# Performance work log

Measured on AMD Instinct MI355X. Metric: run time of the kernel, lower is better.

The kernel has to match this reference:

```python
import jax, jax.numpy as jnp
import numpy as np

IDENTITY_WEIGHT = 0.5
EPS_NORM = 1e-6   # channel RMSNorm eps
EPS_COS = 1e-12   # cosine-sim norm eps (matches torch F.normalize default)


def setup_inputs() -> dict:
    key = jax.random.key(0)
    k1, k2 = jax.random.split(key)
    B, C, H, W = 32, 768, 32, 32
    X = jax.random.normal(k1, (B, C, H, W), dtype=jnp.float32)
    # 1x1 conv weight [out=3C, in=C] (kernel dims squeezed)
    W_in = jax.random.normal(k2, (3 * C, C), dtype=jnp.float32) * (C ** -0.5)
    return {"X": X, "W_in": W_in}


def _cos_sim(t):
    # normalize over the flattened spatial axis (last dim)
    return t / (jnp.linalg.norm(t, axis=-1, keepdims=True) + EPS_COS)


def reference(X, W_in):
    B, C, H, W = X.shape
    # norm: parameter-free RMS over channel dim
    Xn = X * jax.lax.rsqrt(jnp.mean(X * X, axis=1, keepdims=True) + EPS_NORM)
    # 1x1 conv (bias-free) == channel GEMM: [B,3C,H,W]
    qkv = jnp.einsum('oc,bchw->bohw', W_in, Xn)
    K = qkv[:, :C].reshape(B, 1, C, H * W)       # b h c (x y), h=1
    V = qkv[:, C:2 * C].reshape(B, 1, C, H * W)
    # cosine similarity per channel over spatial positions: [B,1,C,1]
    A = jnp.sum(_cos_sim(K) * _cos_sim(V), axis=-1, keepdims=True)
    # affine gate with identity weight (feature_map_attn = identity)
    A = (1.0 - IDENTITY_WEIGHT) * A + IDENTITY_WEIGHT
    A = A.reshape(B, C, 1, 1)  # 'b 1 c 1 -> b c 1 1'
    return A * X
```

## Files before the change

kernel.cpp:

```cpp
#include <hip/hip_runtime.h>
#include <cstdint>
#include <cstddef>


#define B_   32
#define C_   768
#define HW_  1024
#define CHW_ (C_ * HW_)
#define EPS_NORM 1e-6f
#define EPS_COS  1e-12f

using f32x4  = __attribute__((ext_vector_type(4))) float;
using bf16x8 = __attribute__((ext_vector_type(8))) short;

__device__ inline unsigned short f2bf(float f) {
    union { float f; unsigned u; } v; v.f = f;
    unsigned u = v.u;
    u += 0x7fffu + ((u >> 16) & 1u);
    return (unsigned short)(u >> 16);
}

__device__ __forceinline__ void load16_lds(const unsigned short* g, short* l) {
    __builtin_amdgcn_global_load_lds(
        (const __attribute__((address_space(1))) unsigned int*)g,
        (__attribute__((address_space(3))) unsigned int*)l,
        16, 0, 0);
}

__device__ __forceinline__ void stage_half(const unsigned short* g, short* l,
                                           size_t toff, int ldsoff, int rs) {
    load16_lds(g + toff,                     l + ldsoff);
    load16_lds(g + toff + (size_t)rs * 768,  l + ldsoff + 4096);
}

__global__ void wconv_kernel(const float* __restrict__ W, unsigned short* __restrict__ Wst) {
    const int orow = blockIdx.x;
    const int c4   = threadIdx.x;
    const int irow = (orow & 1) * 768 + (orow >> 1);
    const float4 v = reinterpret_cast<const float4*>(W + (size_t)irow * 768)[c4];
    ushort4 o;
    o.x = f2bf(v.x); o.y = f2bf(v.y); o.z = f2bf(v.z); o.w = f2bf(v.w);
    reinterpret_cast<ushort4*>(Wst + (size_t)orow * 768)[c4] = o;
}

__global__ __launch_bounds__(256) void norm_kernel(const float* __restrict__ X,
                                                   unsigned short* __restrict__ Xnt) {
    const int b   = blockIdx.y;
    const int hw0 = blockIdx.x * 64;
    const int tid = threadIdx.x;
    __shared__ float4 P[256];
    __shared__ short  T[64][78];

    const int cg = tid >> 4;
    const int q4 = tid & 15;
    const float* xb = X + (size_t)b * CHW_ + hw0 + q4 * 4;
    float4 s = {0.f, 0.f, 0.f, 0.f};
    #pragma unroll 4
    for (int c = cg; c < 768; c += 16) {
        float4 v = *reinterpret_cast<const float4*>(xb + (size_t)c * HW_);
        s.x += v.x * v.x; s.y += v.y * v.y; s.z += v.z * v.z; s.w += v.w * v.w;
    }
    P[tid] = s;
    __syncthreads();
    if (tid < 16) {
        float4 a = P[tid];
        #pragma unroll
        for (int g = 1; g < 16; ++g) {
            float4 v = P[g * 16 + tid];
            a.x += v.x; a.y += v.y; a.z += v.z; a.w += v.w;
        }
        float4 sc;
        sc.x = rsqrtf(a.x * (1.f / 768.f) + EPS_NORM);
        sc.y = rsqrtf(a.y * (1.f / 768.f) + EPS_NORM);
        sc.z = rsqrtf(a.z * (1.f / 768.f) + EPS_NORM);
        sc.w = rsqrtf(a.w * (1.f / 768.f) + EPS_NORM);
        P[tid] = sc;
    }
    __syncthreads();

    #pragma unroll 1
    for (int ch = 0; ch < 12; ++ch) {
        const int c0 = ch * 64;
        #pragma unroll
        for (int it = 0; it < 4; ++it) {
            int q  = it * 256 + tid;
            int r  = q >> 4;
            int c4 = (q & 15) * 4;
            const float4 x = *reinterpret_cast<const float4*>(
                X + (size_t)b * CHW_ + (size_t)(c0 + r) * HW_ + hw0 + c4);
            const float4 sc = P[q & 15];
            ushort4 o;
            o.x = f2bf(x.x * sc.x); o.y = f2bf(x.y * sc.y);
            o.z = f2bf(x.z * sc.z); o.w = f2bf(x.w * sc.w);
            *reinterpret_cast<ushort4*>(&T[r][c4]) = o;
        }
        __syncthreads();
        #pragma unroll
        for (int it = 0; it < 2; ++it) {
            int q  = it * 256 + tid;
            int rp = q >> 3;
            int cc = (q & 7) * 8;
            __align__(16) unsigned short tmp[8];
            #pragma unroll
            for (int j = 0; j < 8; ++j) tmp[j] = (unsigned short)T[cc + j][rp];
            *reinterpret_cast<uint4*>(
                Xnt + (size_t)b * CHW_ + (size_t)(hw0 + rp) * C_ + c0 + cc) =
                *reinterpret_cast<const uint4*>(tmp);
        }
        __syncthreads();
    }
}

template<int P, bool VM>
__device__ __forceinline__ void phase(const short* Ar, const short* Br,
        const unsigned short* gs, short* ls, size_t toff, int ldsoff, int rs,
        int l15, int wgm64, int wnl64, int slot0, int slot1,
        bf16x8 (&bA)[2][2], bf16x8 (&bB)[4][2], f32x4 (&acc)[8][4]) {
    if constexpr (P == 0) {
        #pragma unroll
        for (int ni = 0; ni < 4; ++ni) {
            const int rB = wnl64 + (ni << 4) + l15;
            bB[ni][0] = *reinterpret_cast<const bf16x8*>(Br + (rB << 6) + slot0);
            bB[ni][1] = *reinterpret_cast<const bf16x8*>(Br + (rB << 6) + slot1);
        }
    }
    #pragma unroll
    for (int s = 0; s < 2; ++s) {
        const int rA = ((((P & 1) << 1) | s) << 4) + l15 + wgm64;
        bA[s][0] = *reinterpret_cast<const bf16x8*>(Ar + (rA << 6) + slot0);
        bA[s][1] = *reinterpret_cast<const bf16x8*>(Ar + (rA << 6) + slot1);
    }
    stage_half(gs, ls, toff, ldsoff, rs);
    if (VM) asm volatile("s_waitcnt vmcnt(6)" ::: "memory");
    __builtin_amdgcn_sched_barrier(0);
    __builtin_amdgcn_s_barrier();
    asm volatile("s_waitcnt lgkmcnt(0)" ::: "memory");
    __builtin_amdgcn_sched_barrier(0);
    __builtin_amdgcn_s_setprio(1);
    #pragma unroll
    for (int s = 0; s < 2; ++s)
        #pragma unroll
        for (int ni = 0; ni < 4; ++ni) {
            acc[(P << 1) | s][ni] = __builtin_amdgcn_mfma_f32_16x16x32_bf16(
                bA[s][0], bB[ni][0], acc[(P << 1) | s][ni], 0, 0, 0);
            acc[(P << 1) | s][ni] = __builtin_amdgcn_mfma_f32_16x16x32_bf16(
                bA[s][1], bB[ni][1], acc[(P << 1) | s][ni], 0, 0, 0);
        }
    __builtin_amdgcn_s_setprio(0);
    __builtin_amdgcn_sched_barrier(0);
    __builtin_amdgcn_s_barrier();
    __builtin_amdgcn_sched_barrier(0);
}

__global__ __launch_bounds__(512, 2) void gemm_kernel(
        const unsigned short* __restrict__ Wst,
        const unsigned short* __restrict__ Xnt,
        float* __restrict__ wsA) {
    const int h     = blockIdx.x;
    const int xcd   = h & 7;
    const int w     = h >> 3;
    const int slice = ((w / 6) << 3) + xcd;
    const int memb  = w % 6;
    const int n0    = (slice & 3) * 256;
    const int c0    = memb * 256;
    const int b     = slice >> 2;

    const int tid  = threadIdx.x;
    const int lane = tid & 63;
    const int wave = tid >> 6;
    const int l15  = lane & 15;
    const int quad = lane >> 4;
    const int wgm64 = (wave >> 2) << 6;
    const int wq    = wave & 3;
    const int wnl64 = (wq & 1) << 6;
    const int hB    = wq >> 1;

    const int lb7   = l15 & 7;
    const int slot0 = (quad ^ lb7) << 3;
    const int slot1 = ((quad + 4) ^ lb7) << 3;

    __shared__ __align__(16) short sA[2][2][128][64];
    __shared__ __align__(16) short sB[2][2][128][64];

    const int r0      = tid >> 3;
    const size_t toff = (size_t)r0 * 768 + (((tid & 7) ^ (r0 & 7)) << 3);
    const int ldsoff  = (r0 & ~7) << 6;

    const unsigned short* Ab = Wst + (size_t)c0 * 768;
    const unsigned short* Bb = Xnt + (size_t)b * CHW_ + (size_t)n0 * 768;

    f32x4 acc[8][4];
    const f32x4 zero = {0.f, 0.f, 0.f, 0.f};
    #pragma unroll
    for (int i = 0; i < 8; ++i)
        #pragma unroll
        for (int j = 0; j < 4; ++j) acc[i][j] = zero;

    bf16x8 bA[2][2], bB[4][2];

    stage_half(Ab,                &sA[0][0][0][0], toff, ldsoff, 128);
    stage_half(Ab + 64 * 768,     &sA[0][1][0][0], toff, ldsoff, 128);
    stage_half(Bb,                &sB[0][0][0][0], toff, ldsoff, 64);
    stage_half(Bb + 128 * 768,    &sB[0][1][0][0], toff, ldsoff, 64);
    stage_half(Bb + 64,           &sB[1][0][0][0], toff, ldsoff, 64);
    stage_half(Bb + 128 * 768 + 64, &sB[1][1][0][0], toff, ldsoff, 64);
    stage_half(Ab + 64,           &sA[1][0][0][0], toff, ldsoff, 128);
    asm volatile("s_waitcnt vmcnt(6)" ::: "memory");
    __builtin_amdgcn_s_barrier();
    __builtin_amdgcn_sched_barrier(0);

    for (int it = 0; it < 6; ++it) {
        const int kT1 = it * 128 + 64;
        int kT2 = it * 128 + 128; if (kT2 >= 768) kT2 -= 768;
        int kT3 = it * 128 + 192; if (kT3 >= 768) kT3 -= 768;

        phase<0, false>(&sA[0][0][0][0], &sB[0][hB][0][0],
                        Ab + 64 * 768 + kT1, &sA[1][1][0][0], toff, ldsoff, 128,
                        l15, wgm64, wnl64, slot0, slot1, bA, bB, acc);
        phase<1, false>(&sA[0][0][0][0], nullptr,
                        Bb + kT2,            &sB[0][0][0][0], toff, ldsoff, 64,
                        l15, wgm64, wnl64, slot0, slot1, bA, bB, acc);
        phase<2, false>(&sA[0][1][0][0], nullptr,
                        Bb + 128 * 768 + kT2, &sB[0][1][0][0], toff, ldsoff, 64,
                        l15, wgm64, wnl64, slot0, slot1, bA, bB, acc);
        phase<3, true >(&sA[0][1][0][0], nullptr,
                        Ab + kT2,            &sA[0][0][0][0], toff, ldsoff, 128,
                        l15, wgm64, wnl64, slot0, slot1, bA, bB, acc);
        phase<0, false>(&sA[1][0][0][0], &sB[1][hB][0][0],
                        Ab + 64 * 768 + kT2, &sA[0][1][0][0], toff, ldsoff, 128,
                        l15, wgm64, wnl64, slot0, slot1, bA, bB, acc);
        phase<1, false>(&sA[1][0][0][0], nullptr,
                        Bb + kT3,            &sB[1][0][0][0], toff, ldsoff, 64,
                        l15, wgm64, wnl64, slot0, slot1, bA, bB, acc);
        phase<2, false>(&sA[1][1][0][0], nullptr,
                        Bb + 128 * 768 + kT3, &sB[1][1][0][0], toff, ldsoff, 64,
                        l15, wgm64, wnl64, slot0, slot1, bA, bB, acc);
        phase<3, true >(&sA[1][1][0][0], nullptr,
                        Ab + kT3,            &sA[1][0][0][0], toff, ldsoff, 128,
                        l15, wgm64, wnl64, slot0, slot1, bA, bB, acc);
    }
    asm volatile("s_waitcnt vmcnt(0)" ::: "memory");

    #pragma unroll
    for (int mi = 0; mi < 8; ++mi) {
        float d0 = 0.f, e0 = 0.f, f0 = 0.f, d1 = 0.f, e1 = 0.f, f1 = 0.f;
        #pragma unroll
        for (int ni = 0; ni < 4; ++ni) {
            f32x4 a = acc[mi][ni];
            d0 += a[0] * a[1]; e0 += a[0] * a[0]; f0 += a[1] * a[1];
            d1 += a[2] * a[3]; e1 += a[2] * a[2]; f1 += a[3] * a[3];
        }
        #pragma unroll
        for (int off = 1; off < 16; off <<= 1) {
            d0 += __shfl_xor(d0, off); e0 += __shfl_xor(e0, off); f0 += __shfl_xor(f0, off);
            d1 += __shfl_xor(d1, off); e1 += __shfl_xor(e1, off); f1 += __shfl_xor(f1, off);
        }
        if (l15 == 0) {
            const int ch = (c0 >> 1) + wgm64 + (mi << 3) + (quad << 1);
            float* dst = wsA + ((size_t)b * C_ + ch) * 3;
            atomicAdd(dst + 0, d0); atomicAdd(dst + 1, e0); atomicAdd(dst + 2, f0);
            atomicAdd(dst + 3, d1); atomicAdd(dst + 4, e1); atomicAdd(dst + 5, f1);
        }
    }
}

__global__ __launch_bounds__(256) void final_kernel(const float* __restrict__ X,
                                                    const float* __restrict__ wsA,
                                                    float* __restrict__ out) {
    const int bc0 = blockIdx.x * 8;
    const int tid = threadIdx.x;
    #pragma unroll
    for (int j = 0; j < 8; ++j) {
        const int bc = bc0 + j;
        const float* a = wsA + (size_t)bc * 3;
        const float pd = a[0], pk = a[1], pv = a[2];
        const float g = 0.5f * (pd / ((sqrtf(pk) + EPS_COS) * (sqrtf(pv) + EPS_COS))) + 0.5f;
        const size_t i4 = (size_t)bc * 256 + tid;
        float4 x = reinterpret_cast<const float4*>(X)[i4];
        float4 o;
        o.x = x.x * g; o.y = x.y * g; o.z = x.z * g; o.w = x.w * g;
        reinterpret_cast<float4*>(out)[i4] = o;
    }
}

extern "C" void kernel_launch(void* const* d_in, const int* in_sizes, int n_in,
                              void* d_out, int out_size, void* d_ws, size_t ws_size,
                              hipStream_t stream) {
    const float* X = (const float*)d_in[0];
    const float* W = (const float*)d_in[1];
    float* out = (float*)d_out;

    char* ws = (char*)d_ws;
    float* wsA           = (float*)ws;
    unsigned short* Wst  = (unsigned short*)(ws + 425984);
    unsigned short* Xnt  = (unsigned short*)(ws + 2785280);

    hipMemsetAsync(ws, 0, 294912, stream);

    wconv_kernel<<<dim3(1536),   192, 0, stream>>>(W, Wst);
    norm_kernel <<<dim3(16, 32), 256, 0, stream>>>(X, Xnt);
    gemm_kernel <<<dim3(768),    512, 0, stream>>>(Wst, Xnt, wsA);
    final_kernel<<<dim3(3072),   256, 0, stream>>>(X, wsA, out);
}
```

Before: 323.6 us.

## Make GEMM blocks persistent over three channel tiles reusing the X tile

Each GEMM block now covers three 256-row weight tiles for one 256-column spatial tile, so 256 blocks replace 768. The pipeline runs continuously across tile boundaries and flushes the partial reductions with atomics after each tile. The aim is to drop per-block prologue and epilogue costs and to raise reuse of the staged X tile. The cost is a grid of 256 blocks at occupancy 1, which may leave CUs underused, and the loss of the XCD-aware block ordering.

```diff
diff --git a/kernel.cpp b/kernel.cpp
--- a/kernel.cpp
+++ b/kernel.cpp
@@ -152,18 +152,40 @@
     __builtin_amdgcn_sched_barrier(0);
 }
 
-__global__ __launch_bounds__(512, 2) void gemm_kernel(
+__device__ __forceinline__ void dump_acc(f32x4 (&acc)[8][4], float* __restrict__ wsA,
+                                         int b, int c0, int wgm64, int quad, int l15) {
+    #pragma unroll
+    for (int mi = 0; mi < 8; ++mi) {
+        float d0 = 0.f, e0 = 0.f, f0 = 0.f, d1 = 0.f, e1 = 0.f, f1 = 0.f;
+        #pragma unroll
+        for (int ni = 0; ni < 4; ++ni) {
+            f32x4 a = acc[mi][ni];
+            d0 += a[0] * a[1]; e0 += a[0] * a[0]; f0 += a[1] * a[1];
+            d1 += a[2] * a[3]; e1 += a[2] * a[2]; f1 += a[3] * a[3];
+            acc[mi][ni] = (f32x4){0.f, 0.f, 0.f, 0.f};
+        }
+        #pragma unroll
+        for (int off = 1; off < 16; off <<= 1) {
+            d0 += __shfl_xor(d0, off); e0 += __shfl_xor(e0, off); f0 += __shfl_xor(f0, off);
+            d1 += __shfl_xor(d1, off); e1 += __shfl_xor(e1, off); f1 += __shfl_xor(f1, off);
+        }
+        if (l15 == 0) {
+            const int ch = (c0 >> 1) + wgm64 + (mi << 3) + (quad << 1);
+            float* dst = wsA + ((size_t)b * C_ + ch) * 3;
+            atomicAdd(dst + 0, d0); atomicAdd(dst + 1, e0); atomicAdd(dst + 2, f0);
+            atomicAdd(dst + 3, d1); atomicAdd(dst + 4, e1); atomicAdd(dst + 5, f1);
+        }
+    }
+}
+
+__global__ __launch_bounds__(512, 1) void gemm_kernel(
         const unsigned short* __restrict__ Wst,
         const unsigned short* __restrict__ Xnt,
         float* __restrict__ wsA) {
-    const int h     = blockIdx.x;
-    const int xcd   = h & 7;
-    const int w     = h >> 3;
-    const int slice = ((w / 6) << 3) + xcd;
-    const int memb  = w % 6;
-    const int n0    = (slice & 3) * 256;
-    const int c0    = memb * 256;
-    const int b     = slice >> 2;
+    const int x     = blockIdx.x;
+    const int n0    = (x >> 1) * 256;
+    const int cbase = (x & 1) * 768;
+    const int b     = blockIdx.y;
 
     const int tid  = threadIdx.x;
     const int lane = tid & 63;
@@ -186,8 +208,16 @@
     const size_t toff = (size_t)r0 * 768 + (((tid & 7) ^ (r0 & 7)) << 3);
     const int ldsoff  = (r0 & ~7) << 6;
 
-    const unsigned short* Ab = Wst + (size_t)c0 * 768;
     const unsigned short* Bb = Xnt + (size_t)b * CHW_ + (size_t)n0 * 768;
+
+    auto Ag = [&](int T) {
+        const int Tc = (T > 35) ? (T - 2) : T;
+        return Wst + (size_t)(cbase + (Tc / 12) * 256) * 768 + (size_t)(Tc % 12) * 64;
+    };
+    auto Bg = [&](int T) {
+        const int Tc = (T > 35) ? (T - 2) : T;
+        return Bb + (size_t)(Tc % 12) * 64;
+    };
 
     f32x4 acc[8][4];
     const f32x4 zero = {0.f, 0.f, 0.f, 0.f};
@@ -198,70 +228,57 @@
 
     bf16x8 bA[2][2], bB[4][2];
 
-    stage_half(Ab,                &sA[0][0][0][0], toff, ldsoff, 128);
-    stage_half(Ab + 64 * 768,     &sA[0][1][0][0], toff, ldsoff, 128);
-    stage_half(Bb,                &sB[0][0][0][0], toff, ldsoff, 64);
-    stage_half(Bb + 128 * 768,    &sB[0][1][0][0], toff, ldsoff, 64);
-    stage_half(Bb + 64,           &sB[1][0][0][0], toff, ldsoff, 64);
-    stage_half(Bb + 128 * 768 + 64, &sB[1][1][0][0], toff, ldsoff, 64);
-    stage_half(Ab + 64,           &sA[1][0][0][0], toff, ldsoff, 128);
+    stage_half(Ag(0),               &sA[0][0][0][0], toff, ldsoff, 128);
+    stage_half(Ag(0) + 64 * 768,    &sA[0][1][0][0], toff, ldsoff, 128);
+    stage_half(Bg(0),               &sB[0][0][0][0], toff, ldsoff, 64);
+    stage_half(Bg(0) + 128 * 768,   &sB[0][1][0][0], toff, ldsoff, 64);
+    stage_half(Bg(1),               &sB[1][0][0][0], toff, ldsoff, 64);
+    stage_half(Bg(1) + 128 * 768,   &sB[1][1][0][0], toff, ldsoff, 64);
+    stage_half(Ag(1),               &sA[1][0][0][0], toff, ldsoff, 128);
     asm volatile("s_waitcnt vmcnt(6)" ::: "memory");
     __builtin_amdgcn_s_barrier();
     __builtin_amdgcn_sched_barrier(0);
 
-    for (int it = 0; it < 6; ++it) {
-        const int kT1 = it * 128 + 64;
-        int kT2 = it * 128 + 128; if (kT2 >= 768) kT2 -= 768;
-        int kT3 = it * 128 + 192; if (kT3 >= 768) kT3 -= 768;
+    #pragma unroll 1
+    for (int t = 0; t < 18; ++t) {
+        const int T1 = 2 * t + 1, T2 = 2 * t + 2, T3 = 2 * t + 3;
+        const unsigned short* A1 = Ag(T1);
+        const unsigned short* A2 = Ag(T2);
+        const unsigned short* A3 = Ag(T3);
+        const unsigned short* B2 = Bg(T2);
+        const unsigned short* B3 = Bg(T3);
 
         phase<0, false>(&sA[0][0][0][0], &sB[0][hB][0][0],
-                        Ab + 64 * 768 + kT1, &sA[1][1][0][0], toff, ldsoff, 128,
+                        A1 + 64 * 768,  &sA[1][1][0][0], toff, ldsoff, 128,
                         l15, wgm64, wnl64, slot0, slot1, bA, bB, acc);
         phase<1, false>(&sA[0][0][0][0], nullptr,
-                        Bb + kT2,            &sB[0][0][0][0], toff, ldsoff, 64,
+                        B2,             &sB[0][0][0][0], toff, ldsoff, 64,
                         l15, wgm64, wnl64, slot0, slot1, bA, bB, acc);
         phase<2, false>(&sA[0][1][0][0], nullptr,
-                        Bb + 128 * 768 + kT2, &sB[0][1][0][0], toff, ldsoff, 64,
+                        B2 + 128 * 768, &sB[0][1][0][0], toff, ldsoff, 64,
                         l15, wgm64, wnl64, slot0, slot1, bA, bB, acc);
         phase<3, true >(&sA[0][1][0][0], nullptr,
-                        Ab + kT2,            &sA[0][0][0][0], toff, ldsoff, 128,
+                        A2,             &sA[0][0][0][0], toff, ldsoff, 128,
                         l15, wgm64, wnl64, slot0, slot1, bA, bB, acc);
         phase<0, false>(&sA[1][0][0][0], &sB[1][hB][0][0],
-                        Ab + 64 * 768 + kT2, &sA[0][1][0][0], toff, ldsoff, 128,
+                        A2 + 64 * 768,  &sA[0][1][0][0], toff, ldsoff, 128,
                         l15, wgm64, wnl64, slot0, slot1, bA, bB, acc);
         phase<1, false>(&sA[1][0][0][0], nullptr,
-                        Bb + kT3,            &sB[1][0][0][0], toff, ldsoff, 64,
+                        B3,             &sB[1][0][0][0], toff, ldsoff, 64,
                         l15, wgm64, wnl64, slot0, slot1, bA, bB, acc);
         phase<2, false>(&sA[1][1][0][0], nullptr,
-                        Bb + 128 * 768 + kT3, &sB[1][1][0][0], toff, ldsoff, 64,
+                        B3 + 128 * 768, &sB[1][1][0][0], toff, ldsoff, 64,
                         l15, wgm64, wnl64, slot0, slot1, bA, bB, acc);
         phase<3, true >(&sA[1][1][0][0], nullptr,
-                        Ab + kT3,            &sA[1][0][0][0], toff, ldsoff, 128,
-                        l15, wgm64, wnl64, slot0, slot1, bA, bB, acc);
+                        A3,             &sA[1][0][0][0], toff, ldsoff, 128,
+                        l15, wgm64, wnl64, slot0, slot1, bA, bB, acc);
+
+        if (t == 5 || t == 11) {
+            dump_acc(acc, wsA, b, cbase + (t / 6) * 256, wgm64, quad, l15);
+        }
     }
     asm volatile("s_waitcnt vmcnt(0)" ::: "memory");
-
-    #pragma unroll
-    for (int mi = 0; mi < 8; ++mi) {
-        float d0 = 0.f, e0 = 0.f, f0 = 0.f, d1 = 0.f, e1 = 0.f, f1 = 0.f;
-        #pragma unroll
-        for (int ni = 0; ni < 4; ++ni) {
-            f32x4 a = acc[mi][ni];
-            d0 += a[0] * a[1]; e0 += a[0] * a[0]; f0 += a[1] * a[1];
-            d1 += a[2] * a[3]; e1 += a[2] * a[2]; f1 += a[3] * a[3];
-        }
-        #pragma unroll
-        for (int off = 1; off < 16; off <<= 1) {
-            d0 += __shfl_xor(d0, off); e0 += __shfl_xor(e0, off); f0 += __shfl_xor(f0, off);
-            d1 += __shfl_xor(d1, off); e1 += __shfl_xor(e1, off); f1 += __shfl_xor(f1, off);
-        }
-        if (l15 == 0) {
-            const int ch = (c0 >> 1) + wgm64 + (mi << 3) + (quad << 1);
-            float* dst = wsA + ((size_t)b * C_ + ch) * 3;
-            atomicAdd(dst + 0, d0); atomicAdd(dst + 1, e0); atomicAdd(dst + 2, f0);
-            atomicAdd(dst + 3, d1); atomicAdd(dst + 4, e1); atomicAdd(dst + 5, f1);
-        }
-    }
+    dump_acc(acc, wsA, b, cbase + 512, wgm64, quad, l15);
 }
 
 __global__ __launch_bounds__(256) void final_kernel(const float* __restrict__ X,
@@ -299,6 +316,6 @@
 
     wconv_kernel<<<dim3(1536),   192, 0, stream>>>(W, Wst);
     norm_kernel <<<dim3(16, 32), 256, 0, stream>>>(X, Xnt);
-    gemm_kernel <<<dim3(768),    512, 0, stream>>>(Wst, Xnt, wsA);
+    gemm_kernel <<<dim3(8, 32),  512, 0, stream>>>(Wst, Xnt, wsA);
     final_kernel<<<dim3(3072),   256, 0, stream>>>(X, wsA, out);
 }
```

Measured after the change: 340.2 us. 5.1% more time.

## Restructure GEMM to keep full-K activation tile resident and stream weights

Applied to the files above, without the earlier changes.

Each GEMM block now owns a 64-position slice of one batch and loads its full-K activation tile into shared memory once. It then streams all weight channel tiles through a double-buffered stage and flushes partial cosine sums after each 256-channel tile. Zeroing of the accumulator workspace moves from a memset into the weight-conversion kernel, which removes one launch. The grid drops to 512 blocks at one block per CU with a larger LDS footprint, and weights are re-read by every block, which may lower occupancy and raise L2 traffic.

```diff
diff --git a/kernel.cpp b/kernel.cpp
--- a/kernel.cpp
+++ b/kernel.cpp
@@ -27,15 +27,17 @@
         16, 0, 0);
 }
 
-__device__ __forceinline__ void stage_half(const unsigned short* g, short* l,
-                                           size_t toff, int ldsoff, int rs) {
-    load16_lds(g + toff,                     l + ldsoff);
-    load16_lds(g + toff + (size_t)rs * 768,  l + ldsoff + 4096);
-}
-
-__global__ void wconv_kernel(const float* __restrict__ W, unsigned short* __restrict__ Wst) {
+#define WAITVM(n) asm volatile("s_waitcnt vmcnt(" #n ")" ::: "memory")
+#define SB0 __builtin_amdgcn_sched_barrier(0)
+
+__global__ void wconv_kernel(const float* __restrict__ W, unsigned short* __restrict__ Wst,
+                             float* __restrict__ wsA) {
     const int orow = blockIdx.x;
     const int c4   = threadIdx.x;
+    if (orow < 96) {
+        const float4 z = {0.f, 0.f, 0.f, 0.f};
+        reinterpret_cast<float4*>(wsA)[orow * 192 + c4] = z;
+    }
     const int irow = (orow & 1) * 768 + (orow >> 1);
     const float4 v = reinterpret_cast<const float4*>(W + (size_t)irow * 768)[c4];
     ushort4 o;
@@ -111,156 +113,159 @@
     }
 }
 
-template<int P, bool VM>
-__device__ __forceinline__ void phase(const short* Ar, const short* Br,
-        const unsigned short* gs, short* ls, size_t toff, int ldsoff, int rs,
-        int l15, int wgm64, int wnl64, int slot0, int slot1,
-        bf16x8 (&bA)[2][2], bf16x8 (&bB)[4][2], f32x4 (&acc)[8][4]) {
-    if constexpr (P == 0) {
-        #pragma unroll
-        for (int ni = 0; ni < 4; ++ni) {
-            const int rB = wnl64 + (ni << 4) + l15;
-            bB[ni][0] = *reinterpret_cast<const bf16x8*>(Br + (rB << 6) + slot0);
-            bB[ni][1] = *reinterpret_cast<const bf16x8*>(Br + (rB << 6) + slot1);
-        }
-    }
-    #pragma unroll
-    for (int s = 0; s < 2; ++s) {
-        const int rA = ((((P & 1) << 1) | s) << 4) + l15 + wgm64;
-        bA[s][0] = *reinterpret_cast<const bf16x8*>(Ar + (rA << 6) + slot0);
-        bA[s][1] = *reinterpret_cast<const bf16x8*>(Ar + (rA << 6) + slot1);
-    }
-    stage_half(gs, ls, toff, ldsoff, rs);
-    if (VM) asm volatile("s_waitcnt vmcnt(6)" ::: "memory");
-    __builtin_amdgcn_sched_barrier(0);
+template<int KT, bool GUARD>
+__device__ __forceinline__ void phase(const short* ArA, const short* BrA,
+        short* st0, short* st1, const unsigned short* srcA,
+        int slot0, int slot1, f32x4 (&acc)[4][2]) {
+    if constexpr (GUARD) { WAITVM(0); }
+    SB0;
     __builtin_amdgcn_s_barrier();
+    SB0;
+    bf16x8 a0[4], a1[4], b0[2], b1[2];
+    const short* Ab = ArA + ((KT & 1) << 14);
+    const short* Bb = BrA + (KT << 12);
+    #pragma unroll
+    for (int n = 0; n < 2; ++n) {
+        b0[n] = *reinterpret_cast<const bf16x8*>(Bb + (n << 10) + slot0);
+        b1[n] = *reinterpret_cast<const bf16x8*>(Bb + (n << 10) + slot1);
+    }
+    #pragma unroll
+    for (int i = 0; i < 4; ++i) {
+        a0[i] = *reinterpret_cast<const bf16x8*>(Ab + (i << 10) + slot0);
+        a1[i] = *reinterpret_cast<const bf16x8*>(Ab + (i << 10) + slot1);
+    }
+    short* st = ((KT + 1) & 1) ? st1 : st0;
+    #pragma unroll
+    for (int j = 0; j < 4; ++j)
+        load16_lds(srcA + j * 49152, st + (j << 12));
     asm volatile("s_waitcnt lgkmcnt(0)" ::: "memory");
-    __builtin_amdgcn_sched_barrier(0);
+    SB0;
     __builtin_amdgcn_s_setprio(1);
     #pragma unroll
-    for (int s = 0; s < 2; ++s)
-        #pragma unroll
-        for (int ni = 0; ni < 4; ++ni) {
-            acc[(P << 1) | s][ni] = __builtin_amdgcn_mfma_f32_16x16x32_bf16(
-                bA[s][0], bB[ni][0], acc[(P << 1) | s][ni], 0, 0, 0);
-            acc[(P << 1) | s][ni] = __builtin_amdgcn_mfma_f32_16x16x32_bf16(
-                bA[s][1], bB[ni][1], acc[(P << 1) | s][ni], 0, 0, 0);
+    for (int i = 0; i < 4; ++i)
+        #pragma unroll
+        for (int n = 0; n < 2; ++n) {
+            acc[i][n] = __builtin_amdgcn_mfma_f32_16x16x32_bf16(a0[i], b0[n], acc[i][n], 0, 0, 0);
+            acc[i][n] = __builtin_amdgcn_mfma_f32_16x16x32_bf16(a1[i], b1[n], acc[i][n], 0, 0, 0);
         }
     __builtin_amdgcn_s_setprio(0);
-    __builtin_amdgcn_sched_barrier(0);
-    __builtin_amdgcn_s_barrier();
-    __builtin_amdgcn_sched_barrier(0);
-}
-
-__global__ __launch_bounds__(512, 2) void gemm_kernel(
+    SB0;
+}
+
+__device__ __forceinline__ void dump_acc(f32x4 (&acc)[4][2], float* __restrict__ wsAb,
+                                         int ct, int wm, int quad, int l15) {
+    #pragma unroll
+    for (int i = 0; i < 4; ++i) {
+        float d0, e0, f0, d1, e1, f1;
+        {
+            f32x4 x = acc[i][0], y = acc[i][1];
+            d0 = x[0]*x[1] + y[0]*y[1]; e0 = x[0]*x[0] + y[0]*y[0]; f0 = x[1]*x[1] + y[1]*y[1];
+            d1 = x[2]*x[3] + y[2]*y[3]; e1 = x[2]*x[2] + y[2]*y[2]; f1 = x[3]*x[3] + y[3]*y[3];
+            acc[i][0] = (f32x4){0.f,0.f,0.f,0.f};
+            acc[i][1] = (f32x4){0.f,0.f,0.f,0.f};
+        }
+        #pragma unroll
+        for (int off = 1; off < 16; off <<= 1) {
+            d0 += __shfl_xor(d0, off); e0 += __shfl_xor(e0, off); f0 += __shfl_xor(f0, off);
+            d1 += __shfl_xor(d1, off); e1 += __shfl_xor(e1, off); f1 += __shfl_xor(f1, off);
+        }
+        if (l15 == 0) {
+            const int ch = ct * 128 + ((wm + 16 * i + 4 * quad) >> 1);
+            float* dst = wsAb + (size_t)ch * 3;
+            atomicAdd(dst + 0, d0); atomicAdd(dst + 1, e0); atomicAdd(dst + 2, f0);
+            atomicAdd(dst + 3, d1); atomicAdd(dst + 4, e1); atomicAdd(dst + 5, f1);
+        }
+    }
+    WAITVM(24);
+    SB0;
+}
+
+template<bool G0>
+__device__ __forceinline__ void ct_body(const short* ArA, const short* BrA,
+        short* st0, short* st1, const unsigned short* Acur,
+        int slot0, int slot1, f32x4 (&acc)[4][2]) {
+    phase< 0, G0  >(ArA, BrA, st0, st1, Acur +  1 * 64, slot0, slot1, acc);
+    phase< 1, true>(ArA, BrA, st0, st1, Acur +  2 * 64, slot0, slot1, acc);
+    phase< 2, true>(ArA, BrA, st0, st1, Acur +  3 * 64, slot0, slot1, acc);
+    phase< 3, true>(ArA, BrA, st0, st1, Acur +  4 * 64, slot0, slot1, acc);
+    phase< 4, true>(ArA, BrA, st0, st1, Acur +  5 * 64, slot0, slot1, acc);
+    phase< 5, true>(ArA, BrA, st0, st1, Acur +  6 * 64, slot0, slot1, acc);
+    phase< 6, true>(ArA, BrA, st0, st1, Acur +  7 * 64, slot0, slot1, acc);
+    phase< 7, true>(ArA, BrA, st0, st1, Acur +  8 * 64, slot0, slot1, acc);
+    phase< 8, true>(ArA, BrA, st0, st1, Acur +  9 * 64, slot0, slot1, acc);
+    phase< 9, true>(ArA, BrA, st0, st1, Acur + 10 * 64, slot0, slot1, acc);
+    phase<10, true>(ArA, BrA, st0, st1, Acur + 11 * 64, slot0, slot1, acc);
+    phase<11, true>(ArA, BrA, st0, st1, Acur + 196608,  slot0, slot1, acc);
+}
+
+__global__ __launch_bounds__(512, 1) void gemm_kernel(
         const unsigned short* __restrict__ Wst,
         const unsigned short* __restrict__ Xnt,
         float* __restrict__ wsA) {
-    const int h     = blockIdx.x;
-    const int xcd   = h & 7;
-    const int w     = h >> 3;
-    const int slice = ((w / 6) << 3) + xcd;
-    const int memb  = w % 6;
-    const int n0    = (slice & 3) * 256;
-    const int c0    = memb * 256;
-    const int b     = slice >> 2;
-
+    const int hw0 = blockIdx.x << 6;
+    const int b   = blockIdx.y;
     const int tid  = threadIdx.x;
     const int lane = tid & 63;
     const int wave = tid >> 6;
     const int l15  = lane & 15;
     const int quad = lane >> 4;
-    const int wgm64 = (wave >> 2) << 6;
-    const int wq    = wave & 3;
-    const int wnl64 = (wq & 1) << 6;
-    const int hB    = wq >> 1;
-
-    const int lb7   = l15 & 7;
+    const int lb7  = l15 & 7;
+    const int wm   = (wave >> 1) << 6;
+    const int wn   = (wave & 1) << 5;
     const int slot0 = (quad ^ lb7) << 3;
     const int slot1 = ((quad + 4) ^ lb7) << 3;
 
-    __shared__ __align__(16) short sA[2][2][128][64];
-    __shared__ __align__(16) short sB[2][2][128][64];
+    __shared__ __align__(16) short sB[12][64][64];
+    __shared__ __align__(16) short sA[2][256][64];
 
     const int r0      = tid >> 3;
-    const size_t toff = (size_t)r0 * 768 + (((tid & 7) ^ (r0 & 7)) << 3);
+    const int chsw    = ((tid & 7) ^ (r0 & 7)) << 3;
+    const size_t toffA = (size_t)r0 * 768 + chsw;
+    const size_t toffB = ((size_t)(b << 10) + hw0 + r0) * 768 + chsw;
     const int ldsoff  = (r0 & ~7) << 6;
 
-    const unsigned short* Ab = Wst + (size_t)c0 * 768;
-    const unsigned short* Bb = Xnt + (size_t)b * CHW_ + (size_t)n0 * 768;
-
-    f32x4 acc[8][4];
-    const f32x4 zero = {0.f, 0.f, 0.f, 0.f};
-    #pragma unroll
-    for (int i = 0; i < 8; ++i)
-        #pragma unroll
-        for (int j = 0; j < 4; ++j) acc[i][j] = zero;
-
-    bf16x8 bA[2][2], bB[4][2];
-
-    stage_half(Ab,                &sA[0][0][0][0], toff, ldsoff, 128);
-    stage_half(Ab + 64 * 768,     &sA[0][1][0][0], toff, ldsoff, 128);
-    stage_half(Bb,                &sB[0][0][0][0], toff, ldsoff, 64);
-    stage_half(Bb + 128 * 768,    &sB[0][1][0][0], toff, ldsoff, 64);
-    stage_half(Bb + 64,           &sB[1][0][0][0], toff, ldsoff, 64);
-    stage_half(Bb + 128 * 768 + 64, &sB[1][1][0][0], toff, ldsoff, 64);
-    stage_half(Ab + 64,           &sA[1][0][0][0], toff, ldsoff, 128);
-    asm volatile("s_waitcnt vmcnt(6)" ::: "memory");
-    __builtin_amdgcn_s_barrier();
-    __builtin_amdgcn_sched_barrier(0);
-
-    for (int it = 0; it < 6; ++it) {
-        const int kT1 = it * 128 + 64;
-        int kT2 = it * 128 + 128; if (kT2 >= 768) kT2 -= 768;
-        int kT3 = it * 128 + 192; if (kT3 >= 768) kT3 -= 768;
-
-        phase<0, false>(&sA[0][0][0][0], &sB[0][hB][0][0],
-                        Ab + 64 * 768 + kT1, &sA[1][1][0][0], toff, ldsoff, 128,
-                        l15, wgm64, wnl64, slot0, slot1, bA, bB, acc);
-        phase<1, false>(&sA[0][0][0][0], nullptr,
-                        Bb + kT2,            &sB[0][0][0][0], toff, ldsoff, 64,
-                        l15, wgm64, wnl64, slot0, slot1, bA, bB, acc);
-        phase<2, false>(&sA[0][1][0][0], nullptr,
-                        Bb + 128 * 768 + kT2, &sB[0][1][0][0], toff, ldsoff, 64,
-                        l15, wgm64, wnl64, slot0, slot1, bA, bB, acc);
-        phase<3, true >(&sA[0][1][0][0], nullptr,
-                        Ab + kT2,            &sA[0][0][0][0], toff, ldsoff, 128,
-                        l15, wgm64, wnl64, slot0, slot1, bA, bB, acc);
-        phase<0, false>(&sA[1][0][0][0], &sB[1][hB][0][0],
-                        Ab + 64 * 768 + kT2, &sA[0][1][0][0], toff, ldsoff, 128,
-                        l15, wgm64, wnl64, slot0, slot1, bA, bB, acc);
-        phase<1, false>(&sA[1][0][0][0], nullptr,
-                        Bb + kT3,            &sB[1][0][0][0], toff, ldsoff, 64,
-                        l15, wgm64, wnl64, slot0, slot1, bA, bB, acc);
-        phase<2, false>(&sA[1][1][0][0], nullptr,
-                        Bb + 128 * 768 + kT3, &sB[1][1][0][0], toff, ldsoff, 64,
-                        l15, wgm64, wnl64, slot0, slot1, bA, bB, acc);
-        phase<3, true >(&sA[1][1][0][0], nullptr,
-                        Ab + kT3,            &sA[1][0][0][0], toff, ldsoff, 128,
-                        l15, wgm64, wnl64, slot0, slot1, bA, bB, acc);
-    }
-    asm volatile("s_waitcnt vmcnt(0)" ::: "memory");
-
-    #pragma unroll
-    for (int mi = 0; mi < 8; ++mi) {
-        float d0 = 0.f, e0 = 0.f, f0 = 0.f, d1 = 0.f, e1 = 0.f, f1 = 0.f;
-        #pragma unroll
-        for (int ni = 0; ni < 4; ++ni) {
-            f32x4 a = acc[mi][ni];
-            d0 += a[0] * a[1]; e0 += a[0] * a[0]; f0 += a[1] * a[1];
-            d1 += a[2] * a[3]; e1 += a[2] * a[2]; f1 += a[3] * a[3];
-        }
-        #pragma unroll
-        for (int off = 1; off < 16; off <<= 1) {
-            d0 += __shfl_xor(d0, off); e0 += __shfl_xor(e0, off); f0 += __shfl_xor(f0, off);
-            d1 += __shfl_xor(d1, off); e1 += __shfl_xor(e1, off); f1 += __shfl_xor(f1, off);
-        }
-        if (l15 == 0) {
-            const int ch = (c0 >> 1) + wgm64 + (mi << 3) + (quad << 1);
-            float* dst = wsA + ((size_t)b * C_ + ch) * 3;
-            atomicAdd(dst + 0, d0); atomicAdd(dst + 1, e0); atomicAdd(dst + 2, f0);
-            atomicAdd(dst + 3, d1); atomicAdd(dst + 4, e1); atomicAdd(dst + 5, f1);
-        }
+    short* st0 = &sA[0][0][0] + ldsoff;
+    short* st1 = &sA[1][0][0] + ldsoff;
+    const short* ArA = &sA[0][0][0] + ((wm + l15) << 6);
+    const short* BrA = &sB[0][0][0] + ((wn + l15) << 6);
+
+    f32x4 acc[4][2];
+    #pragma unroll
+    for (int i = 0; i < 4; ++i) { acc[i][0] = (f32x4){0.f,0.f,0.f,0.f};
+                                  acc[i][1] = (f32x4){0.f,0.f,0.f,0.f}; }
+
+    #pragma unroll
+    for (int kt = 0; kt < 12; ++kt)
+        load16_lds(Xnt + toffB + kt * 64, &sB[kt][0][0] + ldsoff);
+    #pragma unroll
+    for (int j = 0; j < 4; ++j)
+        load16_lds(Wst + toffA + (size_t)j * 49152, st0 + (j << 12));
+
+    float* wsAb = wsA + (size_t)b * (C_ * 3);
+
+    ct_body<true >(ArA, BrA, st0, st1, Wst + toffA,            slot0, slot1, acc);
+    dump_acc(acc, wsAb, 0, wm, quad, l15);
+    #pragma unroll 1
+    for (int ct = 1; ct < 5; ++ct) {
+        ct_body<false>(ArA, BrA, st0, st1, Wst + toffA + (size_t)ct * 196608,
+                       slot0, slot1, acc);
+        dump_acc(acc, wsAb, ct, wm, quad, l15);
+    }
+    {
+        const unsigned short* Acur = Wst + toffA + (size_t)5 * 196608;
+        phase< 0, false>(ArA, BrA, st0, st1, Acur +  1 * 64, slot0, slot1, acc);
+        phase< 1, true >(ArA, BrA, st0, st1, Acur +  2 * 64, slot0, slot1, acc);
+        phase< 2, true >(ArA, BrA, st0, st1, Acur +  3 * 64, slot0, slot1, acc);
+        phase< 3, true >(ArA, BrA, st0, st1, Acur +  4 * 64, slot0, slot1, acc);
+        phase< 4, true >(ArA, BrA, st0, st1, Acur +  5 * 64, slot0, slot1, acc);
+        phase< 5, true >(ArA, BrA, st0, st1, Acur +  6 * 64, slot0, slot1, acc);
+        phase< 6, true >(ArA, BrA, st0, st1, Acur +  7 * 64, slot0, slot1, acc);
+        phase< 7, true >(ArA, BrA, st0, st1, Acur +  8 * 64, slot0, slot1, acc);
+        phase< 8, true >(ArA, BrA, st0, st1, Acur +  9 * 64, slot0, slot1, acc);
+        phase< 9, true >(ArA, BrA, st0, st1, Acur + 10 * 64, slot0, slot1, acc);
+        phase<10, true >(ArA, BrA, st0, st1, Acur + 11 * 64, slot0, slot1, acc);
+        phase<11, true >(ArA, BrA, st0, st1, Acur + 10 * 64, slot0, slot1, acc);
+        dump_acc(acc, wsAb, 5, wm, quad, l15);
     }
 }
 
@@ -295,10 +300,8 @@
     unsigned short* Wst  = (unsigned short*)(ws + 425984);
     unsigned short* Xnt  = (unsigned short*)(ws + 2785280);
 
-    hipMemsetAsync(ws, 0, 294912, stream);
-
-    wconv_kernel<<<dim3(1536),   192, 0, stream>>>(W, Wst);
+    wconv_kernel<<<dim3(1536),   192, 0, stream>>>(W, Wst, wsA);
     norm_kernel <<<dim3(16, 32), 256, 0, stream>>>(X, Xnt);
-    gemm_kernel <<<dim3(768),    512, 0, stream>>>(Wst, Xnt, wsA);
+    gemm_kernel <<<dim3(16, 32), 512, 0, stream>>>(Wst, Xnt, wsA);
     final_kernel<<<dim3(3072),   256, 0, stream>>>(X, wsA, out);
 }
```

After: 435.0 us. 1.34x slower.
